# Kernel tuning notes

Hardware: AMD Instinct MI355X
Metric: run time of the kernel (lower is better)

Reference implementation:

```python
import jax, jax.numpy as jnp
import numpy as np

B, S, D, H = 2, 4096, 768, 12
DH = D // H
SCALE = 1.0 / DH ** 0.5


def setup_inputs() -> dict:
    key = jax.random.key(0)
    k1, k2, k3, k4, k5 = jax.random.split(key, 5)
    x = jax.random.normal(k1, (B, S, D), dtype=jnp.float32)
    # nn.Linear weights: stored as [out, in]; init ~ U(-1/sqrt(in), 1/sqrt(in))
    lim = 1.0 / np.sqrt(D)
    W_qkv = jax.random.uniform(k2, (3 * D, D), minval=-lim, maxval=lim, dtype=jnp.float32)
    b_qkv = jax.random.uniform(k3, (3 * D,), minval=-lim, maxval=lim, dtype=jnp.float32)
    W_out = jax.random.uniform(k4, (D, D), minval=-lim, maxval=lim, dtype=jnp.float32)
    b_out = jax.random.uniform(k5, (D,), minval=-lim, maxval=lim, dtype=jnp.float32)
    return {"x": x, "W_qkv": W_qkv, "b_qkv": b_qkv, "W_out": W_out, "b_out": b_out}


def reference(x, W_qkv, b_qkv, W_out, b_out):
    bs, ns, _ = x.shape
    qkv = x @ W_qkv.T + b_qkv                       # [B, S, 3D]
    qkv = qkv.reshape(bs, ns, 3, H, DH)
    qkv = jnp.transpose(qkv, (2, 0, 3, 1, 4))        # [3, B, H, S, DH]
    q, k, v = qkv[0], qkv[1], qkv[2]
    attn = jnp.einsum('bhqd,bhkd->bhqk', q, k)       # [B, H, S, S]
    attn = jax.nn.softmax(attn * SCALE, axis=-1)
    out = jnp.einsum('bhqk,bhkd->bhqd', attn, v)     # [B, H, S, DH]
    out = jnp.transpose(out, (0, 2, 1, 3)).reshape(bs, ns, D)
    return out @ W_out.T + b_out
```

## Files before the change

kernel.cpp:

```cpp
#include <hip/hip_runtime.h>
#include <hip/hip_bf16.h>
#include <stdint.h>

#define B_    2
#define S_    4096
#define D_    768
#define H_    12
#define DH_   64
#define BH_   (B_*H_)
#define M_    (B_*S_)
#define NQKV_ 2304
#define QSCALE_ 0.18033688011112042f

typedef unsigned short bf16u;
typedef short bf16x8 __attribute__((ext_vector_type(8)));
typedef float f32x4 __attribute__((ext_vector_type(4)));

__device__ __forceinline__ bf16u f2bf(float f) {
    unsigned u = __float_as_uint(f);
    u += 0x7FFFu + ((u >> 16) & 1u);
    return (bf16u)(u >> 16);
}

__device__ __forceinline__ void gl_lds16(const void* g, void* l) {
    __builtin_amdgcn_global_load_lds(
        (const __attribute__((address_space(1))) unsigned*)g,
        (__attribute__((address_space(3))) unsigned*)l, 16, 0, 0);
}

__global__ __launch_bounds__(256) void convert_kernel(
    const float* __restrict__ src, bf16u* __restrict__ dst, int n4)
{
    int i = blockIdx.x * 256 + threadIdx.x;
    if (i < n4) {
        float4 v = ((const float4*)src)[i];
        ushort4 o;
        o.x = f2bf(v.x); o.y = f2bf(v.y); o.z = f2bf(v.z); o.w = f2bf(v.w);
        ((ushort4*)dst)[i] = o;
    }
}

template<int EPI>
__global__ __launch_bounds__(256) void gemm_kernel(
    const bf16u* __restrict__ A, const bf16u* __restrict__ Bw,
    const float* __restrict__ bias, float* __restrict__ Cout,
    bf16u* __restrict__ Qb, bf16u* __restrict__ Kb, bf16u* __restrict__ Vtb)
{
    __shared__ bf16u As[128*32];
    __shared__ bf16u Bs[128*32];
    const int tid  = threadIdx.x;
    const int lane = tid & 63;
    const int wave = tid >> 6;
    const int wr = wave >> 1, wc = wave & 1;
    const int lr = lane & 15;
    const int quad = lane >> 4;

    const int nwg  = gridDim.x * gridDim.y;
    const int fblk = blockIdx.y * gridDim.x + blockIdx.x;
    const int vblk = (fblk & 7) * (nwg >> 3) + (fblk >> 3);
    const int m0 = (vblk / gridDim.x) * 128;
    const int n0 = (vblk % gridDim.x) * 128;

    f32x4 acc[4][4];
    #pragma unroll
    for (int i = 0; i < 4; i++)
        #pragma unroll
        for (int j = 0; j < 4; j++)
            acc[i][j] = (f32x4){0.f, 0.f, 0.f, 0.f};

    for (int k0 = 0; k0 < 768; k0 += 32) {
        #pragma unroll
        for (int r = 0; r < 2; r++) {
            int c = r * 256 + tid;
            int row = c >> 2;
            int col = ((c & 3) ^ (row & 3)) * 8;
            gl_lds16(A  + (size_t)(m0 + row) * 768 + k0 + col, (char*)As + c * 16);
            gl_lds16(Bw + (size_t)(n0 + row) * 768 + k0 + col, (char*)Bs + c * 16);
        }
        __syncthreads();
        bf16x8 af[4], bg[4];
        #pragma unroll
        for (int t = 0; t < 4; t++) {
            int ra = wr * 64 + t * 16 + lr;
            int rb = wc * 64 + t * 16 + lr;
            af[t] = *(const bf16x8*)(As + ra * 32 + ((quad ^ (ra & 3)) * 8));
            bg[t] = *(const bf16x8*)(Bs + rb * 32 + ((quad ^ (rb & 3)) * 8));
        }
        #pragma unroll
        for (int i = 0; i < 4; i++)
            #pragma unroll
            for (int j = 0; j < 4; j++)
                acc[i][j] = __builtin_amdgcn_mfma_f32_16x16x32_bf16(
                    af[i], bg[j], acc[i][j], 0, 0, 0);
        __syncthreads();
    }

    #pragma unroll
    for (int i = 0; i < 4; i++) {
        int mbase = m0 + wr * 64 + i * 16 + quad * 4;
        #pragma unroll
        for (int j = 0; j < 4; j++) {
            int n = n0 + wc * 64 + j * 16 + lr;
            float bv = bias[n];
            if (EPI == 0) {
                #pragma unroll
                for (int r = 0; r < 4; r++)
                    Cout[(size_t)(mbase + r) * 768 + n] = acc[i][j][r] + bv;
            } else {
                int t3  = n / 768;
                int rem = n - t3 * 768;
                int h   = rem >> 6;
                int dh  = rem & 63;
                #pragma unroll
                for (int r = 0; r < 4; r++) {
                    int mm = mbase + r;
                    int b  = mm >> 12;
                    int s  = mm & 4095;
                    int bh = b * H_ + h;
                    float v = acc[i][j][r] + bv;
                    if (t3 == 0)
                        Qb[((size_t)bh * S_ + s) * DH_ + dh] = f2bf(v * QSCALE_);
                    else if (t3 == 1)
                        Kb[((size_t)bh * S_ + s) * DH_ + dh] = f2bf(v);
                    else
                        Vtb[((size_t)bh * DH_ + dh) * S_ + s] = f2bf(v);
                }
            }
        }
    }
}

__global__ __launch_bounds__(512, 6) void attn_kernel(
    const bf16u* __restrict__ Qb, const bf16u* __restrict__ Kb,
    const bf16u* __restrict__ Vtb, bf16u* __restrict__ A2)
{
    __shared__ char Lds[32768];
    const int tid  = threadIdx.x;
    const int lane = tid & 63;
    const int w    = tid >> 6;
    const int lr   = lane & 15;
    const int quad = lane >> 4;

    const int fblk = blockIdx.y * gridDim.x + blockIdx.x;
    const int vblk = (fblk & 7) * 96 + (fblk >> 3);
    const int q0   = (vblk & 31) * 128;
    const int bh   = vblk >> 5;

    const size_t kbase_g = (size_t)bh * S_ * DH_;
    const size_t vbase_g = (size_t)bh * DH_ * S_;

    bf16x8 aq0, aq1;
    {
        const size_t qb = ((size_t)bh * S_ + q0 + w * 16 + lr) * DH_ + quad * 8;
        aq0 = *(const bf16x8*)(Qb + qb);
        aq1 = *(const bf16x8*)(Qb + qb + 32);
    }

    bf16x8 onesf;
    #pragma unroll
    for (int j = 0; j < 8; j++) onesf[j] = (short)0x3F80;

    f32x4 o[4];
    f32x4 l_acc = (f32x4){0.f, 0.f, 0.f, 0.f};
    #pragma unroll
    for (int t = 0; t < 4; t++) o[t] = (f32x4){0.f, 0.f, 0.f, 0.f};

    int kvaddr[4][2];
    #pragma unroll
    for (int nt = 0; nt < 4; nt++) {
        int rk = nt * 16 + lr;
        kvaddr[nt][0] = (rk * 64 + ((quad ^ (rk & 7)) * 8)) * 2;
        kvaddr[nt][1] = (rk * 64 + (((4 + quad) ^ (rk & 7)) * 8)) * 2;
    }

    auto stage = [&](int kv0, int bf) {
        int c = tid;
        int row = c >> 3;
        int col = ((c & 7) ^ (row & 7)) * 8;
        gl_lds16(Kb  + kbase_g + (size_t)(kv0 + row) * DH_ + col,
                 Lds + bf * 8192 + c * 16);
        gl_lds16(Vtb + vbase_g + (size_t)row * S_ + kv0 + col,
                 Lds + 16384 + bf * 8192 + c * 16);
    };

    stage(0, 0);

    auto body = [&](int it, int buf, bool do_stage) __attribute__((always_inline)) {
        __syncthreads();
        if (do_stage) stage((it + 1) * 64, buf ^ 1);

        const char* Kbuf = Lds + buf * 8192;
        const char* Vbuf = Lds + 16384 + buf * 8192;

        f32x4 sc[4];
        __builtin_amdgcn_s_setprio(1);
        #pragma unroll
        for (int nt = 0; nt < 4; nt++) {
            const bf16x8 bk0 = *(const bf16x8*)(Kbuf + kvaddr[nt][0]);
            const bf16x8 bk1 = *(const bf16x8*)(Kbuf + kvaddr[nt][1]);
            f32x4 s = (f32x4){0.f, 0.f, 0.f, 0.f};
            s = __builtin_amdgcn_mfma_f32_16x16x32_bf16(bk0, aq0, s, 0, 0, 0);
            s = __builtin_amdgcn_mfma_f32_16x16x32_bf16(bk1, aq1, s, 0, 0, 0);
            sc[nt] = s;
        }
        __builtin_amdgcn_s_setprio(0);

        unsigned W[4][2];
        #pragma unroll
        for (int nt = 0; nt < 4; nt++) {
            float p0 = __builtin_amdgcn_exp2f(sc[nt][0]);
            float p1 = __builtin_amdgcn_exp2f(sc[nt][1]);
            float p2 = __builtin_amdgcn_exp2f(sc[nt][2]);
            float p3 = __builtin_amdgcn_exp2f(sc[nt][3]);
            W[nt][0] = __builtin_amdgcn_perm(__float_as_uint(p1),
                                             __float_as_uint(p0), 0x07060302u);
            W[nt][1] = __builtin_amdgcn_perm(__float_as_uint(p3),
                                             __float_as_uint(p2), 0x07060302u);
        }

        bf16x8 ap[2];
        #pragma unroll
        for (int ks = 0; ks < 2; ks++) {
            union { unsigned u[4]; bf16x8 v; } Af;
            #pragma unroll
            for (int b = 0; b < 2; b++) {
                auto r1 = __builtin_amdgcn_permlane32_swap(
                    W[2 * ks][b], W[2 * ks + 1][b], false, false);
                auto r2 = __builtin_amdgcn_permlane16_swap(
                    r1[0], r1[1], false, false);
                Af.u[b]     = r2[0];
                Af.u[2 + b] = r2[1];
            }
            ap[ks] = Af.v;
        }

        __builtin_amdgcn_s_setprio(1);
        l_acc = __builtin_amdgcn_mfma_f32_16x16x32_bf16(ap[0], onesf, l_acc, 0, 0, 0);
        l_acc = __builtin_amdgcn_mfma_f32_16x16x32_bf16(ap[1], onesf, l_acc, 0, 0, 0);
        #pragma unroll
        for (int nt = 0; nt < 4; nt++) {
            const bf16x8 bv0 = *(const bf16x8*)(Vbuf + kvaddr[nt][0]);
            const bf16x8 bv1 = *(const bf16x8*)(Vbuf + kvaddr[nt][1]);
            o[nt] = __builtin_amdgcn_mfma_f32_16x16x32_bf16(ap[0], bv0, o[nt], 0, 0, 0);
            o[nt] = __builtin_amdgcn_mfma_f32_16x16x32_bf16(ap[1], bv1, o[nt], 0, 0, 0);
        }
        __builtin_amdgcn_s_setprio(0);
    };

    #pragma unroll 1
    for (int it = 0; it < S_ / 64 - 2; it += 2) {
        body(it,     0, true);
        body(it + 1, 1, true);
    }
    body(S_ / 64 - 2, 0, true);
    body(S_ / 64 - 1, 1, false);

    const int b = bh / H_, h = bh % H_;
    float rl[4];
    #pragma unroll
    for (int r2 = 0; r2 < 4; r2++) rl[r2] = 1.0f / l_acc[r2];
    #pragma unroll
    for (int nt = 0; nt < 4; nt++)
        #pragma unroll
        for (int r2 = 0; r2 < 4; r2++) {
            int q = q0 + w * 16 + quad * 4 + r2;
            float v = o[nt][r2] * rl[r2];
            A2[((size_t)b * S_ + q) * D_ + h * DH_ + nt * 16 + lr] = f2bf(v);
        }
}

extern "C" void kernel_launch(void* const* d_in, const int* in_sizes, int n_in,
                              void* d_out, int out_size, void* d_ws, size_t ws_size,
                              hipStream_t stream) {
    const float* x     = (const float*)d_in[0];
    const float* W_qkv = (const float*)d_in[1];
    const float* b_qkv = (const float*)d_in[2];
    const float* W_out = (const float*)d_in[3];
    const float* b_out = (const float*)d_in[4];
    float* out = (float*)d_out;
    char* ws = (char*)d_ws;

    bf16u* xb    = (bf16u*)(ws + 0);
    bf16u* wqkvb = (bf16u*)(ws + 12582912);
    bf16u* woutb = (bf16u*)(ws + 16121856);
    bf16u* Qb    = (bf16u*)(ws + 17301504);
    bf16u* Kb    = (bf16u*)(ws + 29884416);
    bf16u* Vtb   = (bf16u*)(ws + 42467328);
    bf16u* A2    = (bf16u*)(ws + 55050240);

    convert_kernel<<<6291456/4/256, 256, 0, stream>>>(x, xb, 6291456/4);
    convert_kernel<<<1769472/4/256, 256, 0, stream>>>(W_qkv, wqkvb, 1769472/4);
    convert_kernel<<< 589824/4/256, 256, 0, stream>>>(W_out, woutb, 589824/4);

    dim3 g1(NQKV_/128, M_/128);
    gemm_kernel<1><<<g1, 256, 0, stream>>>(xb, wqkvb, b_qkv, nullptr, Qb, Kb, Vtb);

    dim3 g2(S_/128, BH_);
    attn_kernel<<<g2, 512, 0, stream>>>(Qb, Kb, Vtb, A2);

    dim3 g3(D_/128, M_/128);
    gemm_kernel<0><<<g3, 256, 0, stream>>>(A2, woutb, b_out, out, nullptr, nullptr, nullptr);
}
```

Baseline: 273.2 us.

## Double-buffer GEMM LDS, fuse convert kernels, vectorize V-transpose stores

The three fp32-to-bf16 conversion launches become a single kernel that dispatches on the thread index. The GEMM now double-buffers its LDS tiles so the next K slice is loaded while MFMAs run on the current one, dropping one barrier per iteration, and it raises wave priority around the MFMA block. The QKV epilogue writes the transposed V as packed 4-element bf16 stores instead of scalar stores. This doubles GEMM LDS use, which may lower occupancy.

After: 267.6 us. 1.02x faster.

```diff
diff --git a/kernel.cpp b/kernel.cpp
--- a/kernel.cpp
+++ b/kernel.cpp
@@ -22,22 +22,33 @@
     return (bf16u)(u >> 16);
 }
 
+__device__ __forceinline__ unsigned f2bf_pk(float a, float b) {
+    return (unsigned)f2bf(a) | ((unsigned)f2bf(b) << 16);
+}
+
 __device__ __forceinline__ void gl_lds16(const void* g, void* l) {
     __builtin_amdgcn_global_load_lds(
         (const __attribute__((address_space(1))) unsigned*)g,
         (__attribute__((address_space(3))) unsigned*)l, 16, 0, 0);
 }
 
-__global__ __launch_bounds__(256) void convert_kernel(
-    const float* __restrict__ src, bf16u* __restrict__ dst, int n4)
+#define N1Q_ 1572864
+#define N2Q_  442368
+#define N3Q_  147456
+__global__ __launch_bounds__(256) void convert3_kernel(
+    const float* __restrict__ s1, const float* __restrict__ s2,
+    const float* __restrict__ s3, bf16u* __restrict__ d1,
+    bf16u* __restrict__ d2, bf16u* __restrict__ d3)
 {
     int i = blockIdx.x * 256 + threadIdx.x;
-    if (i < n4) {
-        float4 v = ((const float4*)src)[i];
-        ushort4 o;
-        o.x = f2bf(v.x); o.y = f2bf(v.y); o.z = f2bf(v.z); o.w = f2bf(v.w);
-        ((ushort4*)dst)[i] = o;
-    }
+    const float* s; bf16u* d; int j;
+    if (i < N1Q_)              { s = s1; d = d1; j = i; }
+    else if (i < N1Q_ + N2Q_)  { s = s2; d = d2; j = i - N1Q_; }
+    else                       { s = s3; d = d3; j = i - N1Q_ - N2Q_; }
+    float4 v = ((const float4*)s)[j];
+    ushort4 o;
+    o.x = f2bf(v.x); o.y = f2bf(v.y); o.z = f2bf(v.z); o.w = f2bf(v.w);
+    ((ushort4*)d)[j] = o;
 }
 
 template<int EPI>
@@ -46,8 +57,8 @@
     const float* __restrict__ bias, float* __restrict__ Cout,
     bf16u* __restrict__ Qb, bf16u* __restrict__ Kb, bf16u* __restrict__ Vtb)
 {
-    __shared__ bf16u As[128*32];
-    __shared__ bf16u Bs[128*32];
+    __shared__ bf16u As[2][128*32];
+    __shared__ bf16u Bs[2][128*32];
     const int tid  = threadIdx.x;
     const int lane = tid & 63;
     const int wave = tid >> 6;
@@ -68,32 +79,49 @@
         for (int j = 0; j < 4; j++)
             acc[i][j] = (f32x4){0.f, 0.f, 0.f, 0.f};
 
-    for (int k0 = 0; k0 < 768; k0 += 32) {
+    auto stage = [&](int k0, int bf) {
         #pragma unroll
         for (int r = 0; r < 2; r++) {
             int c = r * 256 + tid;
             int row = c >> 2;
             int col = ((c & 3) ^ (row & 3)) * 8;
-            gl_lds16(A  + (size_t)(m0 + row) * 768 + k0 + col, (char*)As + c * 16);
-            gl_lds16(Bw + (size_t)(n0 + row) * 768 + k0 + col, (char*)Bs + c * 16);
-        }
+            gl_lds16(A  + (size_t)(m0 + row) * 768 + k0 + col,
+                     (char*)&As[bf][0] + c * 16);
+            gl_lds16(Bw + (size_t)(n0 + row) * 768 + k0 + col,
+                     (char*)&Bs[bf][0] + c * 16);
+        }
+    };
+
+    stage(0, 0);
+
+    auto body = [&](int k0, int buf, bool do_stage) __attribute__((always_inline)) {
         __syncthreads();
+        if (do_stage) stage(k0 + 32, buf ^ 1);
         bf16x8 af[4], bg[4];
         #pragma unroll
         for (int t = 0; t < 4; t++) {
             int ra = wr * 64 + t * 16 + lr;
             int rb = wc * 64 + t * 16 + lr;
-            af[t] = *(const bf16x8*)(As + ra * 32 + ((quad ^ (ra & 3)) * 8));
-            bg[t] = *(const bf16x8*)(Bs + rb * 32 + ((quad ^ (rb & 3)) * 8));
-        }
+            af[t] = *(const bf16x8*)(&As[buf][0] + ra * 32 + ((quad ^ (ra & 3)) * 8));
+            bg[t] = *(const bf16x8*)(&Bs[buf][0] + rb * 32 + ((quad ^ (rb & 3)) * 8));
+        }
+        __builtin_amdgcn_s_setprio(1);
         #pragma unroll
         for (int i = 0; i < 4; i++)
             #pragma unroll
             for (int j = 0; j < 4; j++)
                 acc[i][j] = __builtin_amdgcn_mfma_f32_16x16x32_bf16(
                     af[i], bg[j], acc[i][j], 0, 0, 0);
-        __syncthreads();
-    }
+        __builtin_amdgcn_s_setprio(0);
+    };
+
+    #pragma unroll 1
+    for (int k0 = 0; k0 < 768 - 64; k0 += 64) {
+        body(k0,      0, true);
+        body(k0 + 32, 1, true);
+    }
+    body(768 - 64, 0, true);
+    body(768 - 32, 1, false);
 
     #pragma unroll
     for (int i = 0; i < 4; i++) {
@@ -111,19 +139,24 @@
                 int rem = n - t3 * 768;
                 int h   = rem >> 6;
                 int dh  = rem & 63;
-                #pragma unroll
-                for (int r = 0; r < 4; r++) {
-                    int mm = mbase + r;
-                    int b  = mm >> 12;
-                    int s  = mm & 4095;
-                    int bh = b * H_ + h;
-                    float v = acc[i][j][r] + bv;
-                    if (t3 == 0)
-                        Qb[((size_t)bh * S_ + s) * DH_ + dh] = f2bf(v * QSCALE_);
-                    else if (t3 == 1)
-                        Kb[((size_t)bh * S_ + s) * DH_ + dh] = f2bf(v);
-                    else
-                        Vtb[((size_t)bh * DH_ + dh) * S_ + s] = f2bf(v);
+                int b   = mbase >> 12;
+                int s0  = mbase & 4095;
+                int bh  = b * H_ + h;
+                if (t3 == 2) {
+                    uint2 pk;
+                    pk.x = f2bf_pk(acc[i][j][0] + bv, acc[i][j][1] + bv);
+                    pk.y = f2bf_pk(acc[i][j][2] + bv, acc[i][j][3] + bv);
+                    *(uint2*)(Vtb + ((size_t)bh * DH_ + dh) * S_ + s0) = pk;
+                } else if (t3 == 0) {
+                    #pragma unroll
+                    for (int r = 0; r < 4; r++)
+                        Qb[((size_t)bh * S_ + s0 + r) * DH_ + dh] =
+                            f2bf((acc[i][j][r] + bv) * QSCALE_);
+                } else {
+                    #pragma unroll
+                    for (int r = 0; r < 4; r++)
+                        Kb[((size_t)bh * S_ + s0 + r) * DH_ + dh] =
+                            f2bf(acc[i][j][r] + bv);
                 }
             }
         }
@@ -288,9 +321,8 @@
     bf16u* Vtb   = (bf16u*)(ws + 42467328);
     bf16u* A2    = (bf16u*)(ws + 55050240);
 
-    convert_kernel<<<6291456/4/256, 256, 0, stream>>>(x, xb, 6291456/4);
-    convert_kernel<<<1769472/4/256, 256, 0, stream>>>(W_qkv, wqkvb, 1769472/4);
-    convert_kernel<<< 589824/4/256, 256, 0, stream>>>(W_out, woutb, 589824/4);
+    convert3_kernel<<<(N1Q_ + N2Q_ + N3Q_) / 256, 256, 0, stream>>>(
+        x, W_qkv, W_out, xb, wqkvb, woutb);
 
     dim3 g1(NQKV_/128, M_/128);
     gemm_kernel<1><<<g1, 256, 0, stream>>>(xb, wqkvb, b_qkv, nullptr, Qb, Kb, Vtb);
```
